# Optimization experiments

Hardware: AMD Instinct MI355X
Metric: run time of the kernel (lower is better)

Reference implementation:

```python
import jax, jax.numpy as jnp
import numpy as np

HIDDEN = 128
N_NODES = 200000
N_VISITED = 1024


def setup_inputs() -> dict:
    key = jax.random.key(0)
    ks = jax.random.split(key, 7)
    X = jax.random.normal(ks[0], (N_NODES, HIDDEN), dtype=jnp.float32)
    x = jax.random.normal(ks[1], (HIDDEN,), dtype=jnp.float32)
    s = 1.0 / np.sqrt(HIDDEN)
    Wq = jax.random.uniform(ks[2], (3 * HIDDEN, HIDDEN), jnp.float32, -s, s)
    Wk = jax.random.uniform(ks[3], (HIDDEN, HIDDEN), jnp.float32, -s, s)
    Wv = jax.random.uniform(ks[4], (HIDDEN, HIDDEN), jnp.float32, -s, s)
    Wo = jax.random.uniform(ks[5], (HIDDEN, HIDDEN), jnp.float32, -s, s)
    nodes_visited = jax.random.randint(ks[6], (N_VISITED,), 0, N_NODES, dtype=jnp.int32)
    return {
        "X": X, "x": x, "Wq": Wq, "Wk": Wk, "Wv": Wv, "Wo": Wo,
        "nodes_visited": nodes_visited,
        "starting_node": 0, "previous_node": 1,
    }


def reference(X, x, Wq, Wk, Wv, Wo, nodes_visited, starting_node, previous_node):
    # X: [n_nodes, 128]; x: [128]
    n_nodes = X.shape[0]
    # features_concat = [x ; X[start] ; X[prev]]  -> [3*128]
    features_concat = jnp.concatenate([x, X[starting_node], X[previous_node]])
    q = features_concat @ Wq              # [128]
    k = X @ Wk                            # [n_nodes, 128]
    v = X @ Wv                            # [n_nodes, 128]
    u = (k @ q) / jnp.sqrt(jnp.float32(HIDDEN))   # [n_nodes]
    # additive mask: 1 everywhere, 0 at visited nodes (faithful to original)
    mask = jnp.ones((n_nodes,), dtype=X.dtype).at[nodes_visited].set(0.0)
    # final_layer == False branch
    u_ = jax.nn.softmax(u + mask)         # [n_nodes]
    h = u_ @ v                            # [128]
    out = h @ Wo                          # [128]
    return out
```

## Files before the change

kernel.cpp:

```cpp
#include <hip/hip_runtime.h>
#include <math.h>

#define HIDDEN 128
#define MAIN_BLOCKS 512
#define MAIN_THREADS 1024
#define MAX_BMAP_WORDS 6272

__global__ __launch_bounds__(MAIN_THREADS, 8) void stream_kernel(
    const float* __restrict__ X, const float* __restrict__ x,
    const float* __restrict__ Wq, const float* __restrict__ Wk,
    const int* __restrict__ visited, int nv,
    const int* __restrict__ startp, const int* __restrict__ prevp,
    float* __restrict__ Mb, float* __restrict__ Sb, float* __restrict__ Gb,
    int n)
{
    __shared__ unsigned bmap[MAX_BMAP_WORDS];
    __shared__ float fc[384];
    __shared__ float qpart[8][HIDDEN];
    __shared__ float qv[HIDDEN];
    __shared__ float qks[HIDDEN];
    __shared__ float m_arr[32];
    __shared__ float s_arr[32];
    __shared__ float g_all[32 * HIDDEN];

    const int tid  = threadIdx.x;
    const int lane = tid & 63;
    const int sub  = lane & 31;
    const int half = (lane >> 5) & 1;

    const int nwords = (n + 31) >> 5;
    float fcv = 0.f;
    if (tid < 384) {
        if (tid < 128)      fcv = x[tid];
        else if (tid < 256) fcv = X[(size_t)startp[0] * HIDDEN + (tid - 128)];
        else                fcv = X[(size_t)prevp[0]  * HIDDEN + (tid - 256)];
    }
    for (int w = tid; w < nwords; w += MAIN_THREADS) bmap[w] = 0u;
    if (tid < 384) fc[tid] = fcv;
    __syncthreads();

    for (int i = tid; i < nv; i += MAIN_THREADS) {
        const int v = visited[i];
        atomicOr(&bmap[v >> 5], 1u << (v & 31));
    }
    {
        const int col = tid & (HIDDEN - 1);
        const int seg = tid >> 7;
        const int m0  = seg * 48;
        float acc = 0.f;
        #pragma unroll 8
        for (int m = 0; m < 48; ++m)
            acc += fc[m0 + m] * Wq[(size_t)(m0 + m) * HIDDEN + col];
        qpart[seg][col] = acc;
    }
    __syncthreads();
    if (tid < HIDDEN)
        qv[tid] = ((qpart[0][tid] + qpart[1][tid]) + (qpart[2][tid] + qpart[3][tid]))
                + ((qpart[4][tid] + qpart[5][tid]) + (qpart[6][tid] + qpart[7][tid]));
    __syncthreads();

    {
        const int hw0 = tid >> 5;
        const float4 qv4 = *(const float4*)(&qv[sub << 2]);
        #pragma unroll
        for (int k = 0; k < 4; ++k) {
            const int row = hw0 + (k << 5);
            const float4 wk4 = *(const float4*)(Wk + (size_t)row * HIDDEN + (sub << 2));
            float p = wk4.x * qv4.x + wk4.y * qv4.y + wk4.z * qv4.z + wk4.w * qv4.w;
            #pragma unroll
            for (int off = 16; off >= 1; off >>= 1)
                p += __shfl_xor(p, off, 64);
            if (sub == 0) qks[row] = p * 0.08838834764831845f;
        }
    }
    __syncthreads();

    const int wavesPerBlock = MAIN_THREADS >> 6;
    const int gw    = blockIdx.x * wavesPerBlock + (tid >> 6);
    const int rstep = gridDim.x * wavesPerBlock * 8;

    const float4 qkv = *(const float4*)(&qks[sub << 2]);
    const float4 Z   = make_float4(0.f, 0.f, 0.f, 0.f);

    float m = -INFINITY, s = 0.f;
    float g0 = 0.f, g1 = 0.f, g2 = 0.f, g3 = 0.f;

    for (int rb = gw * 8 + half * 4; rb < n; rb += rstep) {
        const int r0 = rb, r1 = rb + 1, r2 = rb + 2, r3 = rb + 3;
        const float4 xv0 = *(const float4*)(X + (size_t)r0 * HIDDEN + (sub << 2));
        const float4 xv1 = (r1 < n) ? *(const float4*)(X + (size_t)r1 * HIDDEN + (sub << 2)) : Z;
        const float4 xv2 = (r2 < n) ? *(const float4*)(X + (size_t)r2 * HIDDEN + (sub << 2)) : Z;
        const float4 xv3 = (r3 < n) ? *(const float4*)(X + (size_t)r3 * HIDDEN + (sub << 2)) : Z;

        float p0 = xv0.x * qkv.x + xv0.y * qkv.y + xv0.z * qkv.z + xv0.w * qkv.w;
        float p1 = xv1.x * qkv.x + xv1.y * qkv.y + xv1.z * qkv.z + xv1.w * qkv.w;
        float p2 = xv2.x * qkv.x + xv2.y * qkv.y + xv2.z * qkv.z + xv2.w * qkv.w;
        float p3 = xv3.x * qkv.x + xv3.y * qkv.y + xv3.z * qkv.z + xv3.w * qkv.w;
        #pragma unroll
        for (int off = 16; off >= 1; off >>= 1) {
            p0 += __shfl_xor(p0, off, 64);
            p1 += __shfl_xor(p1, off, 64);
            p2 += __shfl_xor(p2, off, 64);
            p3 += __shfl_xor(p3, off, 64);
        }
        const float u0 =            p0 + (((bmap[r0 >> 5] >> (r0 & 31)) & 1u) ? 0.f : 1.f);
        const float u1 = (r1 < n) ? p1 + (((bmap[r1 >> 5] >> (r1 & 31)) & 1u) ? 0.f : 1.f) : -INFINITY;
        const float u2 = (r2 < n) ? p2 + (((bmap[r2 >> 5] >> (r2 & 31)) & 1u) ? 0.f : 1.f) : -INFINITY;
        const float u3 = (r3 < n) ? p3 + (((bmap[r3 >> 5] >> (r3 & 31)) & 1u) ? 0.f : 1.f) : -INFINITY;

        const float umax = fmaxf(fmaxf(u0, u1), fmaxf(u2, u3));
        const float mn = fmaxf(m, umax);
        const float sc = __expf(m - mn);
        const float w0 = __expf(u0 - mn);
        const float w1 = __expf(u1 - mn);
        const float w2 = __expf(u2 - mn);
        const float w3 = __expf(u3 - mn);
        s  = s  * sc + ((w0 + w1) + (w2 + w3));
        g0 = g0 * sc + (w0 * xv0.x + w1 * xv1.x) + (w2 * xv2.x + w3 * xv3.x);
        g1 = g1 * sc + (w0 * xv0.y + w1 * xv1.y) + (w2 * xv2.y + w3 * xv3.y);
        g2 = g2 * sc + (w0 * xv0.z + w1 * xv1.z) + (w2 * xv2.z + w3 * xv3.z);
        g3 = g3 * sc + (w0 * xv0.w + w1 * xv1.w) + (w2 * xv2.w + w3 * xv3.w);
        m  = mn;
    }

    const int hw = tid >> 5;
    *(float4*)(&g_all[hw * HIDDEN + (sub << 2)]) = make_float4(g0, g1, g2, g3);
    if (sub == 0) { m_arr[hw] = m; s_arr[hw] = s; }
    __syncthreads();

    float mb = m_arr[0];
    #pragma unroll
    for (int h = 1; h < 32; ++h) mb = fmaxf(mb, m_arr[h]);

    if (tid < HIDDEN) {
        float G = 0.f;
        #pragma unroll 4
        for (int h = 0; h < 32; ++h)
            G += g_all[h * HIDDEN + tid] * __expf(m_arr[h] - mb);
        Gb[blockIdx.x * HIDDEN + tid] = G;
    } else if (tid == HIDDEN) {
        float S = 0.f;
        #pragma unroll
        for (int h = 0; h < 32; ++h) S += s_arr[h] * __expf(m_arr[h] - mb);
        Sb[blockIdx.x] = S;
        Mb[blockIdx.x] = mb;
    }
}

__global__ __launch_bounds__(MAIN_THREADS) void finish_kernel(
    const float* __restrict__ Mb, const float* __restrict__ Sb,
    const float* __restrict__ Gb,
    const float* __restrict__ Wv, const float* __restrict__ Wo,
    float* __restrict__ out)
{
    __shared__ float red[MAIN_THREADS];
    __shared__ float e[MAIN_BLOCKS];
    __shared__ float part[8][HIDDEN];
    __shared__ float pvec[HIDDEN];
    __shared__ float hvec[HIDDEN];

    const int tid = threadIdx.x;
    const int col = tid & (HIDDEN - 1);
    const int seg = tid >> 7;

    const float mt = (tid < MAIN_BLOCKS) ? Mb[tid] : -INFINITY;
    red[tid] = mt; __syncthreads();
    for (int st = 512; st >= 1; st >>= 1) {
        if (tid < st) red[tid] = fmaxf(red[tid], red[tid + st]);
        __syncthreads();
    }
    const float M = red[0];
    __syncthreads();

    float ls = 0.f;
    if (tid < MAIN_BLOCKS) {
        const float eb = __expf(mt - M); e[tid] = eb; ls = Sb[tid] * eb;
    }
    red[tid] = ls; __syncthreads();
    for (int st = 512; st >= 1; st >>= 1) {
        if (tid < st) red[tid] += red[tid + st];
        __syncthreads();
    }
    const float S = red[0];
    __syncthreads();

    {
        const int b0 = seg * (MAIN_BLOCKS / 8);
        float acc = 0.f;
        #pragma unroll 8
        for (int b = 0; b < MAIN_BLOCKS / 8; ++b)
            acc += Gb[(size_t)(b0 + b) * HIDDEN + col] * e[b0 + b];
        part[seg][col] = acc;
    }
    __syncthreads();
    if (tid < HIDDEN)
        pvec[tid] = (((part[0][tid] + part[1][tid]) + (part[2][tid] + part[3][tid]))
                   + ((part[4][tid] + part[5][tid]) + (part[6][tid] + part[7][tid]))) / S;
    __syncthreads();

    {
        const int m0 = seg * 16;
        float acc = 0.f;
        #pragma unroll
        for (int m2 = 0; m2 < 16; ++m2)
            acc += pvec[m0 + m2] * Wv[(size_t)(m0 + m2) * HIDDEN + col];
        part[seg][col] = acc;
    }
    __syncthreads();
    if (tid < HIDDEN)
        hvec[tid] = ((part[0][tid] + part[1][tid]) + (part[2][tid] + part[3][tid]))
                  + ((part[4][tid] + part[5][tid]) + (part[6][tid] + part[7][tid]));
    __syncthreads();

    {
        const int m0 = seg * 16;
        float acc = 0.f;
        #pragma unroll
        for (int m2 = 0; m2 < 16; ++m2)
            acc += hvec[m0 + m2] * Wo[(size_t)(m0 + m2) * HIDDEN + col];
        part[seg][col] = acc;
    }
    __syncthreads();
    if (tid < HIDDEN)
        out[tid] = ((part[0][tid] + part[1][tid]) + (part[2][tid] + part[3][tid]))
                 + ((part[4][tid] + part[5][tid]) + (part[6][tid] + part[7][tid]));
}

extern "C" void kernel_launch(void* const* d_in, const int* in_sizes, int n_in,
                              void* d_out, int out_size, void* d_ws, size_t ws_size,
                              hipStream_t stream)
{
    const float* X       = (const float*)d_in[0];
    const float* x       = (const float*)d_in[1];
    const float* Wq      = (const float*)d_in[2];
    const float* Wk      = (const float*)d_in[3];
    const float* Wv      = (const float*)d_in[4];
    const float* Wo      = (const float*)d_in[5];
    const int*   visited = (const int*)d_in[6];
    const int*   startp  = (const int*)d_in[7];
    const int*   prevp   = (const int*)d_in[8];

    const int n  = in_sizes[0] / HIDDEN;
    const int nv = in_sizes[6];

    float* ws = (float*)d_ws;
    float* Mb = ws + 128;
    float* Sb = Mb + MAIN_BLOCKS;
    float* Gb = Sb + MAIN_BLOCKS;

    stream_kernel<<<MAIN_BLOCKS, MAIN_THREADS, 0, stream>>>(
        X, x, Wq, Wk, visited, nv, startp, prevp, Mb, Sb, Gb, n);
    finish_kernel<<<1, MAIN_THREADS, 0, stream>>>(
        Mb, Sb, Gb, Wv, Wo, (float*)d_out);
}
```

Before: 182.1 us.

## Split query and visited-bitmap prep into a separate kernel before streaming

After: 183.9 us. Within noise of the previous version (+1.0%).

```diff
diff --git a/kernel.cpp b/kernel.cpp
--- a/kernel.cpp
+++ b/kernel.cpp
@@ -6,43 +6,36 @@
 #define MAIN_THREADS 1024
 #define MAX_BMAP_WORDS 6272
 
-__global__ __launch_bounds__(MAIN_THREADS, 8) void stream_kernel(
+__global__ __launch_bounds__(MAIN_THREADS) void prep_kernel(
     const float* __restrict__ X, const float* __restrict__ x,
     const float* __restrict__ Wq, const float* __restrict__ Wk,
     const int* __restrict__ visited, int nv,
     const int* __restrict__ startp, const int* __restrict__ prevp,
-    float* __restrict__ Mb, float* __restrict__ Sb, float* __restrict__ Gb,
-    int n)
-{
-    __shared__ unsigned bmap[MAX_BMAP_WORDS];
+    float* __restrict__ qk, unsigned* __restrict__ bmap_g)
+{
+    const int tid = threadIdx.x;
+
+    if (blockIdx.x == 1) {
+        for (int w = tid; w < MAX_BMAP_WORDS; w += MAIN_THREADS) bmap_g[w] = 0u;
+        __syncthreads();
+        for (int i = tid; i < nv; i += MAIN_THREADS) {
+            const int v = visited[i];
+            atomicOr(&bmap_g[v >> 5], 1u << (v & 31));
+        }
+        return;
+    }
+
     __shared__ float fc[384];
     __shared__ float qpart[8][HIDDEN];
     __shared__ float qv[HIDDEN];
-    __shared__ float qks[HIDDEN];
-    __shared__ float m_arr[32];
-    __shared__ float s_arr[32];
-    __shared__ float g_all[32 * HIDDEN];
-
-    const int tid  = threadIdx.x;
-    const int lane = tid & 63;
-    const int sub  = lane & 31;
-    const int half = (lane >> 5) & 1;
-
-    const int nwords = (n + 31) >> 5;
-    float fcv = 0.f;
+
     if (tid < 384) {
-        if (tid < 128)      fcv = x[tid];
-        else if (tid < 256) fcv = X[(size_t)startp[0] * HIDDEN + (tid - 128)];
-        else                fcv = X[(size_t)prevp[0]  * HIDDEN + (tid - 256)];
-    }
-    for (int w = tid; w < nwords; w += MAIN_THREADS) bmap[w] = 0u;
-    if (tid < 384) fc[tid] = fcv;
-    __syncthreads();
-
-    for (int i = tid; i < nv; i += MAIN_THREADS) {
-        const int v = visited[i];
-        atomicOr(&bmap[v >> 5], 1u << (v & 31));
-    }
+        if (tid < 128)      fc[tid] = x[tid];
+        else if (tid < 256) fc[tid] = X[(size_t)startp[0] * HIDDEN + (tid - 128)];
+        else                fc[tid] = X[(size_t)prevp[0]  * HIDDEN + (tid - 256)];
+    }
+    __syncthreads();
+
     {
         const int col = tid & (HIDDEN - 1);
         const int seg = tid >> 7;
@@ -60,6 +53,7 @@
     __syncthreads();
 
     {
+        const int sub = tid & 31;
         const int hw0 = tid >> 5;
         const float4 qv4 = *(const float4*)(&qv[sub << 2]);
         #pragma unroll
@@ -70,16 +64,31 @@
             #pragma unroll
             for (int off = 16; off >= 1; off >>= 1)
                 p += __shfl_xor(p, off, 64);
-            if (sub == 0) qks[row] = p * 0.08838834764831845f;
+            if (sub == 0) qk[row] = p * 0.08838834764831845f;
         }
     }
-    __syncthreads();
+}
+
+__global__ __launch_bounds__(MAIN_THREADS, 8) void stream_kernel(
+    const float* __restrict__ X, const float* __restrict__ qk,
+    const unsigned* __restrict__ bmap,
+    float* __restrict__ Mb, float* __restrict__ Sb, float* __restrict__ Gb,
+    int n)
+{
+    __shared__ float m_arr[32];
+    __shared__ float s_arr[32];
+    __shared__ float g_all[32 * HIDDEN];
+
+    const int tid  = threadIdx.x;
+    const int lane = tid & 63;
+    const int sub  = lane & 31;
+    const int half = (lane >> 5) & 1;
 
     const int wavesPerBlock = MAIN_THREADS >> 6;
     const int gw    = blockIdx.x * wavesPerBlock + (tid >> 6);
     const int rstep = gridDim.x * wavesPerBlock * 8;
 
-    const float4 qkv = *(const float4*)(&qks[sub << 2]);
+    const float4 qkv = *(const float4*)(qk + (sub << 2));
     const float4 Z   = make_float4(0.f, 0.f, 0.f, 0.f);
 
     float m = -INFINITY, s = 0.f;
@@ -244,12 +253,16 @@
     const int nv = in_sizes[6];
 
     float* ws = (float*)d_ws;
-    float* Mb = ws + 128;
-    float* Sb = Mb + MAIN_BLOCKS;
-    float* Gb = Sb + MAIN_BLOCKS;
-
+    float*    qk     = ws;
+    float*    Mb     = ws + 128;
+    float*    Sb     = Mb + MAIN_BLOCKS;
+    float*    Gb     = Sb + MAIN_BLOCKS;
+    unsigned* bmap_g = (unsigned*)(Gb + (size_t)MAIN_BLOCKS * HIDDEN);
+
+    prep_kernel<<<2, MAIN_THREADS, 0, stream>>>(
+        X, x, Wq, Wk, visited, nv, startp, prevp, qk, bmap_g);
     stream_kernel<<<MAIN_BLOCKS, MAIN_THREADS, 0, stream>>>(
-        X, x, Wq, Wk, visited, nv, startp, prevp, Mb, Sb, Gb, n);
+        X, qk, bmap_g, Mb, Sb, Gb, n);
     finish_kernel<<<1, MAIN_THREADS, 0, stream>>>(
         Mb, Sb, Gb, Wv, Wo, (float*)d_out);
 }
```
